# Kernel optimization log

Hardware: AMD Instinct MI355X
Metric: run time of the kernel (lower is better)

Reference implementation:

```python
import jax, jax.numpy as jnp
import numpy as np

D_MODEL = 2048
H_TOTAL = 32
D_HEAD = D_MODEL // H_TOTAL  # 64
H_ACTIVE = 4
ROPE_BASE = 10000.0


def _apply_rope(t, cos, sin):
    # t: [B, H, T, DH]; cos/sin: [T, DH//2]; interleaved pair rotation
    t1 = t[..., 0::2]
    t2 = t[..., 1::2]
    r1 = t1 * cos - t2 * sin
    r2 = t1 * sin + t2 * cos
    return jnp.stack([r1, r2], axis=-1).reshape(t.shape)


def setup_inputs() -> dict:
    key = jax.random.key(0)
    ks = jax.random.split(key, 4)
    x = jax.random.normal(ks[0], (4, 1024, D_MODEL), dtype=jnp.float32)
    w_router = jax.random.normal(ks[1], (D_MODEL, H_TOTAL), dtype=jnp.float32) * 0.02
    w_qkv = jax.random.normal(ks[2], (D_MODEL, 3 * D_MODEL), dtype=jnp.float32) * 0.02
    w_out = jax.random.normal(ks[3], (D_MODEL, D_MODEL), dtype=jnp.float32) * 0.02
    return {"x": x, "w_router": w_router, "w_qkv": w_qkv, "w_out": w_out}


def reference(x, w_router, w_qkv, w_out):
    B, T, _ = x.shape
    # --- SwitchRouter: per-token probabilities over heads ---
    probs = jax.nn.softmax(x @ w_router, axis=-1)            # [B, T, H]
    # top-h_active heads per token (dense-math equivalent of sparse dispatch)
    _, top_idx = jax.lax.top_k(probs, H_ACTIVE)              # [B, T, HA]
    mask = jnp.sum(jax.nn.one_hot(top_idx, H_TOTAL, dtype=x.dtype), axis=-2)  # [B, T, H]
    gate = probs * mask                                      # router-scored gate

    # --- QKV projection ---
    qkv = x @ w_qkv                                          # [B, T, 3D]
    q, k, v = jnp.split(qkv, 3, axis=-1)
    def to_heads(t):
        return t.reshape(B, T, H_TOTAL, D_HEAD).transpose(0, 2, 1, 3)  # [B, H, T, DH]
    q, k, v = to_heads(q), to_heads(k), to_heads(v)

    # --- RoPE ---
    inv_freq = 1.0 / (ROPE_BASE ** (jnp.arange(0, D_HEAD, 2, dtype=jnp.float32) / D_HEAD))
    ang = jnp.arange(T, dtype=jnp.float32)[:, None] * inv_freq[None, :]  # [T, DH/2]
    cos, sin = jnp.cos(ang), jnp.sin(ang)
    q = _apply_rope(q, cos, sin)
    k = _apply_rope(k, cos, sin)

    # --- causal SDPA ---
    scores = jnp.einsum('bhqd,bhkd->bhqk', q, k) / np.float32(np.sqrt(D_HEAD))
    causal = jnp.tril(jnp.ones((T, T), dtype=bool))
    scores = jnp.where(causal, scores, jnp.finfo(scores.dtype).min)
    attn = jax.nn.softmax(scores, axis=-1)
    out = jnp.einsum('bhqk,bhkd->bhqd', attn, v)             # [B, H, T, DH]

    # --- gate: only active heads contribute (scatter-back equivalent) ---
    out = out * gate.transpose(0, 2, 1)[..., None]           # [B, H, T, DH]
    out = out.transpose(0, 2, 1, 3).reshape(B, T, D_MODEL)
    return out @ w_out
```

## Files before the change

kernel.cpp:

```cpp
#include <hip/hip_runtime.h>
#include <hip/hip_bf16.h>
#include <stdint.h>
#include <stddef.h>

typedef __attribute__((ext_vector_type(8))) short bf16x8;
typedef __attribute__((ext_vector_type(8))) unsigned short u16x8;
typedef __attribute__((ext_vector_type(4))) float f32x4;
typedef __attribute__((ext_vector_type(16))) float f32x16;

#define TT 1024

__device__ __forceinline__ unsigned short f2bf(float f){
  unsigned u = __builtin_bit_cast(unsigned, f);
  unsigned r = 0x7fffu + ((u >> 16) & 1u);
  return (unsigned short)((u + r) >> 16);
}
__device__ __forceinline__ float bf2f(unsigned short s){
  unsigned u = ((unsigned)s) << 16;
  return __builtin_bit_cast(float, u);
}
__device__ __forceinline__ void gload16(const unsigned short* g, unsigned short* l){
  __builtin_amdgcn_global_load_lds(
      (const __attribute__((address_space(1))) void*)g,
      (__attribute__((address_space(3))) void*)l, 16, 0, 0);
}

#define MFMA32(a, b, c) __builtin_amdgcn_mfma_f32_32x32x16_bf16((a), (b), (c), 0, 0, 0)
#define MFMA_B16(a, b, c) __builtin_amdgcn_mfma_f32_16x16x32_bf16((a), (b), (c), 0, 0, 0)

__global__ void transpose_w_kernel(const float* __restrict__ wqkv, const float* __restrict__ wout,
                                   unsigned short* __restrict__ wqkvT, unsigned short* __restrict__ woutT){
  __shared__ float tile[32][33];
  const float* in; unsigned short* out; int C;
  int bx = blockIdx.x;
  if (bx < 192){ in = wqkv; out = wqkvT; C = 6144; }
  else         { in = wout; out = woutT; C = 2048; bx -= 192; }
  const int R = 2048;
  int c0 = bx * 32, r0 = blockIdx.y * 32;
  for (int i = threadIdx.y; i < 32; i += 8)
    tile[i][threadIdx.x] = in[(size_t)(r0 + i) * C + c0 + threadIdx.x];
  __syncthreads();
  for (int i = threadIdx.y; i < 32; i += 8)
    out[(size_t)(c0 + i) * R + r0 + threadIdx.x] = f2bf(tile[threadIdx.x][i]);
}

__global__ __launch_bounds__(256) void prep_kernel(const float* __restrict__ x,
                                                   const float* __restrict__ wr,
                                                   unsigned short* __restrict__ x_bf,
                                                   float* __restrict__ gate,
                                                   unsigned char* __restrict__ heads4,
                                                   float* __restrict__ tab){
  __shared__ float xc[8 * 256];
  __shared__ float red[8 * 8 * 32];
  const int tid = threadIdx.x;
  const int tok0 = blockIdx.x * 8;
  const int p = tid >> 5, h = tid & 31;

  if (blockIdx.x < 128){
    int i2 = blockIdx.x * 256 + tid;
    int pos = i2 >> 5, ii = i2 & 31;
    float freq = powf(10000.0f, -(float)ii / 32.0f);
    float ang = (float)pos * freq;
    tab[i2 * 2]     = cosf(ang);
    tab[i2 * 2 + 1] = sinf(ang);
  }

  float acc[8] = {0.f,0.f,0.f,0.f,0.f,0.f,0.f,0.f};
  for (int kb = 0; kb < 8; kb++){
    __syncthreads();
    {
      int tok = tid >> 5, e = (tid & 31) * 8;
      const float* xp = x + (size_t)(tok0 + tok) * 2048 + kb * 256 + e;
      float4 v0 = *(const float4*)xp, v1 = *(const float4*)(xp + 4);
      float vals[8] = {v0.x, v0.y, v0.z, v0.w, v1.x, v1.y, v1.z, v1.w};
      u16x8 ob;
      #pragma unroll
      for (int jj = 0; jj < 8; jj++) ob[jj] = f2bf(vals[jj]);
      *(u16x8*)(x_bf + (size_t)(tok0 + tok) * 2048 + kb * 256 + e) = ob;
      #pragma unroll
      for (int jj = 0; jj < 8; jj++) xc[tok * 256 + e + jj] = vals[jj];
    }
    __syncthreads();
    const float* wp = wr + (size_t)(kb * 256 + p * 32) * 32 + h;
    #pragma unroll 4
    for (int j = 0; j < 32; j++){
      float wv = wp[j * 32];
      #pragma unroll
      for (int tok = 0; tok < 8; tok++)
        acc[tok] += xc[tok * 256 + p * 32 + j] * wv;
    }
  }
  #pragma unroll
  for (int tok = 0; tok < 8; tok++) red[(p * 8 + tok) * 32 + h] = acc[tok];
  __syncthreads();
  {
    int lane = tid & 63;
    int tok = (tid >> 6) * 2 + (lane >> 5);
    int hh = lane & 31;
    float logit = 0.f;
    #pragma unroll
    for (int pp = 0; pp < 8; pp++) logit += red[(pp * 8 + tok) * 32 + hh];
    float m = logit;
    #pragma unroll
    for (int s = 16; s >= 1; s >>= 1) m = fmaxf(m, __shfl_xor(m, s));
    float e = __expf(logit - m);
    float sum = e;
    #pragma unroll
    for (int s = 16; s >= 1; s >>= 1) sum += __shfl_xor(sum, s);
    float prob = e / sum;
    float v = logit; int sel = 0;
    #pragma unroll
    for (int rr2 = 0; rr2 < 4; rr2++){
      float bv = v; int bi = hh;
      #pragma unroll
      for (int s = 16; s >= 1; s >>= 1){
        float ov = __shfl_xor(bv, s); int oi = __shfl_xor(bi, s);
        if (ov > bv || (ov == bv && oi < bi)) { bv = ov; bi = oi; }
      }
      if (hh == bi) { sel = 1; v = -3.4e38f; }
    }
    gate[(size_t)(tok0 + tok) * 32 + hh] = sel ? prob : 0.f;
    unsigned long long bal = __ballot(sel != 0);
    unsigned selmask = (unsigned)(bal >> ((lane >> 5) * 32));
    if (sel){
      int r = __popc(selmask & ((1u << hh) - 1u));
      heads4[(size_t)(tok0 + tok) * 4 + r] = (unsigned char)hh;
    }
  }
}

__global__ void compact_kernel(const unsigned char* __restrict__ heads4,
                               unsigned short* __restrict__ idx, int* __restrict__ counts){
  int bh = blockIdx.x;
  int b = bh >> 5, h = bh & 31;
  int lane = threadIdx.x;
  int base = 0;
  for (int c = 0; c < 16; c++){
    int t = c * 64 + lane;
    unsigned u = ((const unsigned*)heads4)[b * 1024 + t];
    int r = -1;
    if (((u      ) & 255) == (unsigned)h) r = 0;
    else if (((u >>  8) & 255) == (unsigned)h) r = 1;
    else if (((u >> 16) & 255) == (unsigned)h) r = 2;
    else if (((u >> 24) & 255) == (unsigned)h) r = 3;
    bool act = (r >= 0);
    unsigned long long mask = __ballot(act);
    int pos = base + __popcll(mask & ((1ull << lane) - 1ull));
    if (act) idx[bh * 1024 + pos] = (unsigned short)(t | (r << 10));
    base += __popcll(mask);
  }
  if (lane == 0) counts[bh] = base;
}

__global__ __launch_bounds__(256) void qgemm_kernel(const unsigned short* __restrict__ x_bf,
                                                    const unsigned short* __restrict__ wqkvT,
                                                    const unsigned short* __restrict__ idx,
                                                    const int* __restrict__ counts,
                                                    const float* __restrict__ tab,
                                                    unsigned short* __restrict__ qact){
  __shared__ float red[4][64][64];
  const int bh = blockIdx.x, qt = blockIdx.y;
  const int count = counts[bh];
  if (qt * 64 >= count) return;
  const int b = bh >> 5, h = bh & 31;
  const int tid = threadIdx.x, lane = tid & 63, w = tid >> 6;
  const int li = lane & 15, lg = lane >> 4;
  const int nvalid = min(64, count - qt * 64);
  const unsigned short* myidx = idx + bh * 1024 + qt * 64;

  int atok[4];
  #pragma unroll
  for (int ai = 0; ai < 4; ai++){
    int s = ai * 16 + li;
    atok[ai] = (s < nvalid) ? (myidx[s] & 1023) : 0;
  }
  const unsigned short* Bbase = wqkvT + (size_t)(h * 64) * 2048;

  f32x4 acc[4][4];
  #pragma unroll
  for (int i = 0; i < 4; i++)
    #pragma unroll
    for (int j = 0; j < 4; j++) acc[i][j] = f32x4{0.f, 0.f, 0.f, 0.f};

  const int k0w = w * 512;
  #pragma unroll 2
  for (int ks = 0; ks < 16; ks++){
    int k0 = k0w + ks * 32 + lg * 8;
    bf16x8 af[4], bw[4];
    #pragma unroll
    for (int ai = 0; ai < 4; ai++)
      af[ai] = *(const bf16x8*)(x_bf + (size_t)(b * 1024 + atok[ai]) * 2048 + k0);
    #pragma unroll
    for (int ni = 0; ni < 4; ni++)
      bw[ni] = *(const bf16x8*)(Bbase + (size_t)(ni * 16 + li) * 2048 + k0);
    #pragma unroll
    for (int ai = 0; ai < 4; ai++)
      #pragma unroll
      for (int ni = 0; ni < 4; ni++)
        acc[ai][ni] = MFMA_B16(af[ai], bw[ni], acc[ai][ni]);
  }
  #pragma unroll
  for (int ai = 0; ai < 4; ai++)
    #pragma unroll
    for (int ni = 0; ni < 4; ni++)
      #pragma unroll
      for (int rr = 0; rr < 4; rr++)
        red[w][ai * 16 + lg * 4 + rr][ni * 16 + li] = acc[ai][ni][rr];
  __syncthreads();

  int q = tid >> 2, dbase = (tid & 3) * 16;
  if (q < nvalid){
    int e = myidx[q];
    int tok = e & 1023, r = e >> 10;
    unsigned short* op = qact + ((size_t)((b << 10) + tok) * 4 + r) * 64;
    const float* tp = tab + ((size_t)tok * 32 + (dbase >> 1)) * 2;
    #pragma unroll
    for (int p = 0; p < 8; p++){
      int d0 = dbase + 2 * p;
      float v0 = red[0][q][d0] + red[1][q][d0] + red[2][q][d0] + red[3][q][d0];
      float v1 = red[0][q][d0 + 1] + red[1][q][d0 + 1] + red[2][q][d0 + 1] + red[3][q][d0 + 1];
      float c = tp[2 * p], s = tp[2 * p + 1];
      op[d0]     = f2bf(v0 * c - v1 * s);
      op[d0 + 1] = f2bf(v0 * s + v1 * c);
    }
  }
}

template<int MREP, int EPI>
__global__ __launch_bounds__(256, 2) void gemmk(const unsigned short* __restrict__ A,
                                                const unsigned short* __restrict__ Bt,
                                                float* __restrict__ Cf,
                                                unsigned short* __restrict__ kbuf,
                                                unsigned short* __restrict__ vt,
                                                const float* __restrict__ tab,
                                                int N, int K, int nbm){
  extern __shared__ unsigned short smem[];
  constexpr int BM = MREP * 64;
  constexpr int AU = MREP * 2048;
  constexpr int SLOT = AU + 4096;
  const int nblk = gridDim.x;
  const int raw = blockIdx.x;
  const int tile = (raw & 7) * (nblk >> 3) + (raw >> 3);
  const int bn = tile / nbm, bm = tile % nbm;

  const int tid = threadIdx.x, lane = tid & 63, wid = tid >> 6;
  const int wrow = wid >> 1, wcol = wid & 1;
  const int l31 = lane & 31, hi = lane >> 5;
  const int X = ((l31 >> 1) & 7) << 4;

  const unsigned short* gA[MREP];
  const unsigned short* gB[2];
  #pragma unroll
  for (int p = 0; p < MREP; p++){
    int L = tid * 16 + p * 4096;
    int line = L >> 7;
    int cs = (L & 127) ^ ((line & 7) << 4);
    gA[p] = A + (size_t)(bm * BM + line * 2 + (cs >> 6)) * K + ((cs & 63) >> 1);
  }
  #pragma unroll
  for (int p = 0; p < 2; p++){
    int L = tid * 16 + p * 4096;
    int line = L >> 7;
    int cs = (L & 127) ^ ((line & 7) << 4);
    gB[p] = Bt + (size_t)(bn * 128 + line * 2 + (cs >> 6)) * K + ((cs & 63) >> 1);
  }

  f32x16 acc[MREP][2];
  #pragma unroll
  for (int i = 0; i < MREP; i++)
    #pragma unroll
    for (int j = 0; j < 2; j++) acc[i][j] = f32x16{0,0,0,0,0,0,0,0,0,0,0,0,0,0,0,0};

  const int NT = K >> 5;
  #pragma unroll
  for (int tt = 0; tt < 2; tt++){
    unsigned short* sb = smem + tt * SLOT;
    #pragma unroll
    for (int p = 0; p < MREP; p++) gload16(gA[p] + (size_t)tt * 32, sb + tid * 8 + p * 2048);
    #pragma unroll
    for (int p = 0; p < 2; p++)    gload16(gB[p] + (size_t)tt * 32, sb + AU + tid * 8 + p * 2048);
  }

  for (int t = 0; t < NT; ++t){
    if (t < NT - 1){
      if constexpr (MREP == 4) asm volatile("s_waitcnt vmcnt(6)" ::: "memory");
      else                     asm volatile("s_waitcnt vmcnt(4)" ::: "memory");
    } else                     asm volatile("s_waitcnt vmcnt(0)" ::: "memory");
    __builtin_amdgcn_s_barrier();
    __builtin_amdgcn_sched_barrier(0);
    const unsigned short* bs = smem + (t % 3) * SLOT;
    unsigned short* ns = smem + ((t + 2) % 3) * SLOT;
    const bool st = (t + 2 < NT);
    #pragma unroll
    for (int ks = 0; ks < 2; ks++){
      const int bo = (((l31 & 1) * 64 + ks * 32 + hi * 16) ^ X) >> 1;
      bf16x8 av[MREP], bv[2];
      #pragma unroll
      for (int i = 0; i < MREP; i++)
        av[i] = *(const bf16x8*)(bs + (wrow * (MREP * 16) + i * 16 + (l31 >> 1)) * 64 + bo);
      #pragma unroll
      for (int j = 0; j < 2; j++)
        bv[j] = *(const bf16x8*)(bs + AU + (wcol * 32 + j * 16 + (l31 >> 1)) * 64 + bo);
      if (st){
        if (ks == 0){
          #pragma unroll
          for (int p = 0; p < MREP / 2 + 1; p++)
            gload16(gA[p] + (size_t)(t + 2) * 32, ns + tid * 8 + p * 2048);
        } else {
          #pragma unroll
          for (int p = MREP / 2 + 1; p < MREP; p++)
            gload16(gA[p] + (size_t)(t + 2) * 32, ns + tid * 8 + p * 2048);
          #pragma unroll
          for (int p = 0; p < 2; p++)
            gload16(gB[p] + (size_t)(t + 2) * 32, ns + AU + tid * 8 + p * 2048);
        }
      }
      #pragma unroll
      for (int i = 0; i < MREP; i++){
        acc[i][0] = MFMA32(av[i], bv[0], acc[i][0]);
        acc[i][1] = MFMA32(av[i], bv[1], acc[i][1]);
      }
    }
  }

  if constexpr (EPI == 1){
    if (bn < 16){
      #pragma unroll
      for (int i = 0; i < MREP; i++){
        #pragma unroll
        for (int j = 0; j < 2; j++){
          int col = bn * 128 + wcol * 64 + j * 32 + l31;
          int ii = (col & 63) >> 1;
          #pragma unroll
          for (int g = 0; g < 4; g++){
            #pragma unroll
            for (int rr = 0; rr < 4; rr++){
              int row = bm * BM + wrow * (BM / 2) + i * 32 + g * 8 + hi * 4 + rr;
              int pos = row & (TT - 1);
              const float* tp = tab + ((size_t)pos * 32 + ii) * 2;
              float c = tp[0], s = tp[1];
              float val = acc[i][j][g * 4 + rr];
              float pv = __shfl_xor(val, 1);
              float res = (lane & 1) ? (pv * s + val * c) : (val * c - pv * s);
              kbuf[(size_t)row * 2048 + col] = f2bf(res);
            }
          }
        }
      }
    } else {
      #pragma unroll
      for (int i = 0; i < MREP; i++){
        #pragma unroll
        for (int j = 0; j < 2; j++){
          int vcol = bn * 128 + wcol * 64 + j * 32 + l31 - 2048;
          int hh = vcol >> 6, d = vcol & 63;
          int row0 = bm * BM + wrow * (BM / 2) + i * 32 + hi * 4;
          int b = row0 >> 10, t0 = row0 & (TT - 1);
          #pragma unroll
          for (int g = 0; g < 4; g++){
            ushort4 pk;
            pk.x = f2bf(acc[i][j][g * 4 + 0]); pk.y = f2bf(acc[i][j][g * 4 + 1]);
            pk.z = f2bf(acc[i][j][g * 4 + 2]); pk.w = f2bf(acc[i][j][g * 4 + 3]);
            *(ushort4*)(vt + ((size_t)((b * 32 + hh) * 64 + d)) * TT + t0 + g * 8) = pk;
          }
        }
      }
    }
  } else {
    #pragma unroll
    for (int i = 0; i < MREP; i++){
      #pragma unroll
      for (int j = 0; j < 2; j++){
        int col = bn * 128 + wcol * 64 + j * 32 + l31;
        #pragma unroll
        for (int g = 0; g < 4; g++){
          #pragma unroll
          for (int rr = 0; rr < 4; rr++){
            size_t row = (size_t)(bm * BM + wrow * (BM / 2) + i * 32 + g * 8 + hi * 4 + rr);
            Cf[row * N + col] = acc[i][j][g * 4 + rr];
          }
        }
      }
    }
  }
}

__global__ __launch_bounds__(256) void attn_sparse_kernel(const unsigned short* __restrict__ qact,
                                                          const unsigned short* __restrict__ kbuf,
                                                          const unsigned short* __restrict__ vt,
                                                          const float* __restrict__ gate,
                                                          const unsigned short* __restrict__ idx,
                                                          const int* __restrict__ counts,
                                                          unsigned short* __restrict__ attn_out){
  __shared__ unsigned short Ks[64 * 64];
  __shared__ unsigned short Vs[64 * 64];
  __shared__ unsigned short Ps[4][16 * 64];
  const int bh = blockIdx.x, qt = blockIdx.y;
  const int count = counts[bh];
  if (qt * 64 >= count) return;
  const int b = bh >> 5, h = bh & 31;
  const int tid = threadIdx.x, lane = tid & 63, w = tid >> 6;
  const int li = lane & 15, lg = lane >> 4;
  const unsigned short* myidx = idx + bh * 1024 + qt * 64;
  const int nvalid = min(64, count - qt * 64);
  const int qmax = myidx[nvalid - 1] & 1023;

  int qi[4];
  #pragma unroll
  for (int r = 0; r < 4; r++){
    int s = w * 16 + lg * 4 + r;
    qi[r] = (s < nvalid) ? (myidx[s] & 1023) : -1;
  }
  bf16x8 qf0, qf1;
  {
    int s = w * 16 + li;
    int e2 = (s < nvalid) ? myidx[s] : 0;
    const unsigned short* qp = qact + ((size_t)((b << 10) + (e2 & 1023)) * 4 + (e2 >> 10)) * 64;
    qf0 = *(const bf16x8*)(qp + lg * 8);
    qf1 = *(const bf16x8*)(qp + 32 + lg * 8);
  }
  f32x4 o[4];
  #pragma unroll
  for (int i = 0; i < 4; i++) o[i] = f32x4{0.f, 0.f, 0.f, 0.f};
  float m_run[4], l_run[4];
  #pragma unroll
  for (int r = 0; r < 4; r++){ m_run[r] = -1e30f; l_run[r] = 0.f; }

  const int nkt = (qmax >> 6) + 1;
  for (int kt = 0; kt < nkt; kt++){
    const int kb = kt * 64;
    #pragma unroll
    for (int s2 = 0; s2 < 2; s2++){
      int s = s2 * 256 + tid;
      int r = s >> 3, c = (s & 7) * 8;
      gload16(kbuf + (size_t)(b * TT + kb + r) * 2048 + h * 64 + c, &Ks[s * 8]);
      gload16(vt + (size_t)(bh * 64 + r) * TT + kb + c, &Vs[s * 8]);
    }
    __syncthreads();

    f32x4 s4[4];
    #pragma unroll
    for (int ni = 0; ni < 4; ni++){
      bf16x8 k0 = *(const bf16x8*)(&Ks[(ni * 16 + li) * 64 + lg * 8]);
      bf16x8 k1 = *(const bf16x8*)(&Ks[(ni * 16 + li) * 64 + 32 + lg * 8]);
      f32x4 t = f32x4{0.f, 0.f, 0.f, 0.f};
      t = MFMA_B16(qf0, k0, t);
      t = MFMA_B16(qf1, k1, t);
      s4[ni] = t;
    }
    float mt[4];
    #pragma unroll
    for (int r = 0; r < 4; r++) mt[r] = -1e30f;
    #pragma unroll
    for (int ni = 0; ni < 4; ni++){
      int kidx = kb + ni * 16 + li;
      #pragma unroll
      for (int r = 0; r < 4; r++){
        float val = s4[ni][r] * 0.125f;
        val = (kidx <= qi[r]) ? val : -1e30f;
        s4[ni][r] = val;
        mt[r] = fmaxf(mt[r], val);
      }
    }
    #pragma unroll
    for (int r = 0; r < 4; r++){
      #pragma unroll
      for (int sh = 8; sh >= 1; sh >>= 1) mt[r] = fmaxf(mt[r], __shfl_xor(mt[r], sh));
      float mnew = fmaxf(m_run[r], mt[r]);
      float corr = __expf(m_run[r] - mnew);
      m_run[r] = mnew;
      l_run[r] *= corr;
      #pragma unroll
      for (int j = 0; j < 4; j++) o[j][r] *= corr;
    }
    float rs[4] = {0.f, 0.f, 0.f, 0.f};
    #pragma unroll
    for (int ni = 0; ni < 4; ni++)
      #pragma unroll
      for (int r = 0; r < 4; r++){
        float p = __expf(s4[ni][r] - m_run[r]);
        s4[ni][r] = p;
        rs[r] += p;
      }
    #pragma unroll
    for (int r = 0; r < 4; r++){
      #pragma unroll
      for (int sh = 8; sh >= 1; sh >>= 1) rs[r] += __shfl_xor(rs[r], sh);
      l_run[r] += rs[r];
    }
    #pragma unroll
    for (int ni = 0; ni < 4; ni++)
      #pragma unroll
      for (int r = 0; r < 4; r++)
        Ps[w][(lg * 4 + r) * 64 + ni * 16 + li] = f2bf(s4[ni][r]);
    #pragma unroll
    for (int ks = 0; ks < 2; ks++){
      bf16x8 pa = *(const bf16x8*)(&Ps[w][li * 64 + ks * 32 + lg * 8]);
      #pragma unroll
      for (int ni = 0; ni < 4; ni++){
        bf16x8 vb = *(const bf16x8*)(&Vs[(ni * 16 + li) * 64 + ks * 32 + lg * 8]);
        o[ni] = MFMA_B16(pa, vb, o[ni]);
      }
    }
    __syncthreads();
  }
  #pragma unroll
  for (int r = 0; r < 4; r++){
    if (qi[r] < 0) continue;
    float g = gate[(size_t)(b * TT + qi[r]) * 32 + h];
    float inv = g / l_run[r];
    #pragma unroll
    for (int ni = 0; ni < 4; ni++)
      attn_out[(size_t)(b * TT + qi[r]) * 2048 + h * 64 + ni * 16 + li] = f2bf(o[ni][r] * inv);
  }
}

extern "C" void kernel_launch(void* const* d_in, const int* in_sizes, int n_in,
                              void* d_out, int out_size, void* d_ws, size_t ws_size,
                              hipStream_t stream){
  const float* x        = (const float*)d_in[0];
  const float* w_router = (const float*)d_in[1];
  const float* w_qkv    = (const float*)d_in[2];
  const float* w_out    = (const float*)d_in[3];
  float* out = (float*)d_out;
  char* ws = (char*)d_ws;

  unsigned short* kbuf   = (unsigned short*)(ws);
  unsigned short* vt     = (unsigned short*)(ws + 16777216);
  unsigned short* qact   = (unsigned short*)(ws + 33554432);
  unsigned short* idx    = (unsigned short*)(ws + 37748736);
  int* counts            = (int*)(ws + 38010880);
  unsigned char* heads4  = (unsigned char*)(ws + 38011392);
  unsigned short* x_bf   = (unsigned short*)(ws + 50331648);
  unsigned short* wqkvT  = (unsigned short*)(ws + 67108864);
  unsigned short* woutT  = (unsigned short*)(ws + 92274688);
  float* gate            = (float*)(ws + 100663296);
  float* tab             = (float*)(ws + 101187584);
  unsigned short* attn   = x_bf;

  constexpr int KV_LDS  = 3 * (4 * 4096 + 8192) * 2 / 2;
  (void)hipFuncSetAttribute(reinterpret_cast<const void*>(&gemmk<4, 1>),
                            hipFuncAttributeMaxDynamicSharedMemorySize, KV_LDS);
  (void)hipFuncSetAttribute(reinterpret_cast<const void*>(&gemmk<4, 0>),
                            hipFuncAttributeMaxDynamicSharedMemorySize, KV_LDS);

  hipLaunchKernelGGL(transpose_w_kernel, dim3(256, 64), dim3(32, 8), 0, stream, w_qkv, w_out, wqkvT, woutT);
  hipLaunchKernelGGL(prep_kernel, dim3(512), dim3(256), 0, stream, x, w_router, x_bf, gate, heads4, tab);
  hipLaunchKernelGGL(compact_kernel, dim3(128), dim3(64), 0, stream, heads4, idx, counts);
  hipLaunchKernelGGL((gemmk<4, 1>), dim3(512), dim3(256), KV_LDS, stream,
                     x_bf, wqkvT + (size_t)2048 * 2048, (float*)nullptr, kbuf, vt, tab, 4096, 2048, 16);
  hipLaunchKernelGGL(qgemm_kernel, dim3(128, 16), dim3(256), 0, stream,
                     x_bf, wqkvT, idx, counts, tab, qact);
  (void)hipMemsetAsync(attn, 0, (size_t)4096 * 2048 * 2, stream);
  hipLaunchKernelGGL(attn_sparse_kernel, dim3(128, 16), dim3(256), 0, stream,
                     qact, kbuf, vt, gate, idx, counts, attn);
  hipLaunchKernelGGL((gemmk<4, 0>), dim3(256), dim3(256), KV_LDS, stream,
                     attn, woutT, out, (unsigned short*)nullptr, (unsigned short*)nullptr,
                     (const float*)nullptr, 2048, 2048, 16);
}
```

Measured before the change: 260.6 us.

## Replace dense output projection with sparse per-head GEMM and rank-partial reduce

The dense output projection over the full zero-padded attention buffer, together with its memset, is replaced. Attention results are now written in place into the compact qact buffer. A new kernel multiplies each active head's 64-wide slice by the matching W_out columns and writes bf16 partials into four rank-indexed buffers. A reduce kernel then sums those into the fp32 output. This skips the work for inactive heads (4 of 32) but adds the traffic of writing four bf16 partial tensors and reading them back, plus an extra rounding to bf16 before the sum.

Result: no change. 259.7 us (-0.3%).

```diff
diff --git a/kernel.cpp b/kernel.cpp
--- a/kernel.cpp
+++ b/kernel.cpp
@@ -226,15 +226,14 @@
   }
 }
 
-template<int MREP, int EPI>
 __global__ __launch_bounds__(256, 2) void gemmk(const unsigned short* __restrict__ A,
                                                 const unsigned short* __restrict__ Bt,
-                                                float* __restrict__ Cf,
                                                 unsigned short* __restrict__ kbuf,
                                                 unsigned short* __restrict__ vt,
                                                 const float* __restrict__ tab,
-                                                int N, int K, int nbm){
+                                                int K, int nbm){
   extern __shared__ unsigned short smem[];
+  constexpr int MREP = 4;
   constexpr int BM = MREP * 64;
   constexpr int AU = MREP * 2048;
   constexpr int SLOT = AU + 4096;
@@ -282,10 +281,8 @@
   }
 
   for (int t = 0; t < NT; ++t){
-    if (t < NT - 1){
-      if constexpr (MREP == 4) asm volatile("s_waitcnt vmcnt(6)" ::: "memory");
-      else                     asm volatile("s_waitcnt vmcnt(4)" ::: "memory");
-    } else                     asm volatile("s_waitcnt vmcnt(0)" ::: "memory");
+    if (t < NT - 1) asm volatile("s_waitcnt vmcnt(6)" ::: "memory");
+    else            asm volatile("s_waitcnt vmcnt(0)" ::: "memory");
     __builtin_amdgcn_s_barrier();
     __builtin_amdgcn_sched_barrier(0);
     const unsigned short* bs = smem + (t % 3) * SLOT;
@@ -304,12 +301,10 @@
       if (st){
         if (ks == 0){
           #pragma unroll
-          for (int p = 0; p < MREP / 2 + 1; p++)
+          for (int p = 0; p < 3; p++)
             gload16(gA[p] + (size_t)(t + 2) * 32, ns + tid * 8 + p * 2048);
         } else {
-          #pragma unroll
-          for (int p = MREP / 2 + 1; p < MREP; p++)
-            gload16(gA[p] + (size_t)(t + 2) * 32, ns + tid * 8 + p * 2048);
+          gload16(gA[3] + (size_t)(t + 2) * 32, ns + tid * 8 + 3 * 2048);
           #pragma unroll
           for (int p = 0; p < 2; p++)
             gload16(gB[p] + (size_t)(t + 2) * 32, ns + AU + tid * 8 + p * 2048);
@@ -323,75 +318,56 @@
     }
   }
 
-  if constexpr (EPI == 1){
-    if (bn < 16){
-      #pragma unroll
-      for (int i = 0; i < MREP; i++){
-        #pragma unroll
-        for (int j = 0; j < 2; j++){
-          int col = bn * 128 + wcol * 64 + j * 32 + l31;
-          int ii = (col & 63) >> 1;
-          #pragma unroll
-          for (int g = 0; g < 4; g++){
-            #pragma unroll
-            for (int rr = 0; rr < 4; rr++){
-              int row = bm * BM + wrow * (BM / 2) + i * 32 + g * 8 + hi * 4 + rr;
-              int pos = row & (TT - 1);
-              const float* tp = tab + ((size_t)pos * 32 + ii) * 2;
-              float c = tp[0], s = tp[1];
-              float val = acc[i][j][g * 4 + rr];
-              float pv = __shfl_xor(val, 1);
-              float res = (lane & 1) ? (pv * s + val * c) : (val * c - pv * s);
-              kbuf[(size_t)row * 2048 + col] = f2bf(res);
-            }
-          }
-        }
-      }
-    } else {
-      #pragma unroll
-      for (int i = 0; i < MREP; i++){
-        #pragma unroll
-        for (int j = 0; j < 2; j++){
-          int vcol = bn * 128 + wcol * 64 + j * 32 + l31 - 2048;
-          int hh = vcol >> 6, d = vcol & 63;
-          int row0 = bm * BM + wrow * (BM / 2) + i * 32 + hi * 4;
-          int b = row0 >> 10, t0 = row0 & (TT - 1);
-          #pragma unroll
-          for (int g = 0; g < 4; g++){
-            ushort4 pk;
-            pk.x = f2bf(acc[i][j][g * 4 + 0]); pk.y = f2bf(acc[i][j][g * 4 + 1]);
-            pk.z = f2bf(acc[i][j][g * 4 + 2]); pk.w = f2bf(acc[i][j][g * 4 + 3]);
-            *(ushort4*)(vt + ((size_t)((b * 32 + hh) * 64 + d)) * TT + t0 + g * 8) = pk;
-          }
-        }
-      }
-    }
-  } else {
+  if (bn < 16){
     #pragma unroll
     for (int i = 0; i < MREP; i++){
       #pragma unroll
       for (int j = 0; j < 2; j++){
         int col = bn * 128 + wcol * 64 + j * 32 + l31;
+        int ii = (col & 63) >> 1;
         #pragma unroll
         for (int g = 0; g < 4; g++){
           #pragma unroll
           for (int rr = 0; rr < 4; rr++){
-            size_t row = (size_t)(bm * BM + wrow * (BM / 2) + i * 32 + g * 8 + hi * 4 + rr);
-            Cf[row * N + col] = acc[i][j][g * 4 + rr];
+            int row = bm * BM + wrow * (BM / 2) + i * 32 + g * 8 + hi * 4 + rr;
+            int pos = row & (TT - 1);
+            const float* tp = tab + ((size_t)pos * 32 + ii) * 2;
+            float c = tp[0], s = tp[1];
+            float val = acc[i][j][g * 4 + rr];
+            float pv = __shfl_xor(val, 1);
+            float res = (lane & 1) ? (pv * s + val * c) : (val * c - pv * s);
+            kbuf[(size_t)row * 2048 + col] = f2bf(res);
           }
         }
       }
     }
-  }
-}
-
-__global__ __launch_bounds__(256) void attn_sparse_kernel(const unsigned short* __restrict__ qact,
+  } else {
+    #pragma unroll
+    for (int i = 0; i < MREP; i++){
+      #pragma unroll
+      for (int j = 0; j < 2; j++){
+        int vcol = bn * 128 + wcol * 64 + j * 32 + l31 - 2048;
+        int hh = vcol >> 6, d = vcol & 63;
+        int row0 = bm * BM + wrow * (BM / 2) + i * 32 + hi * 4;
+        int b = row0 >> 10, t0 = row0 & (TT - 1);
+        #pragma unroll
+        for (int g = 0; g < 4; g++){
+          ushort4 pk;
+          pk.x = f2bf(acc[i][j][g * 4 + 0]); pk.y = f2bf(acc[i][j][g * 4 + 1]);
+          pk.z = f2bf(acc[i][j][g * 4 + 2]); pk.w = f2bf(acc[i][j][g * 4 + 3]);
+          *(ushort4*)(vt + ((size_t)((b * 32 + hh) * 64 + d)) * TT + t0 + g * 8) = pk;
+        }
+      }
+    }
+  }
+}
+
+__global__ __launch_bounds__(256) void attn_sparse_kernel(unsigned short* __restrict__ qact,
                                                           const unsigned short* __restrict__ kbuf,
                                                           const unsigned short* __restrict__ vt,
                                                           const float* __restrict__ gate,
                                                           const unsigned short* __restrict__ idx,
-                                                          const int* __restrict__ counts,
-                                                          unsigned short* __restrict__ attn_out){
+                                                          const int* __restrict__ counts){
   __shared__ unsigned short Ks[64 * 64];
   __shared__ unsigned short Vs[64 * 64];
   __shared__ unsigned short Ps[4][16 * 64];
@@ -509,10 +485,102 @@
     if (qi[r] < 0) continue;
     float g = gate[(size_t)(b * TT + qi[r]) * 32 + h];
     float inv = g / l_run[r];
+    int e = myidx[w * 16 + lg * 4 + r];
+    unsigned short* op = qact + ((size_t)((b << 10) + (e & 1023)) * 4 + (e >> 10)) * 64;
     #pragma unroll
     for (int ni = 0; ni < 4; ni++)
-      attn_out[(size_t)(b * TT + qi[r]) * 2048 + h * 64 + ni * 16 + li] = f2bf(o[ni][r] * inv);
-  }
+      op[ni * 16 + li] = f2bf(o[ni][r] * inv);
+  }
+}
+
+__global__ __launch_bounds__(256) void outsp_kernel(const unsigned short* __restrict__ qact,
+                                                    const unsigned short* __restrict__ woutT,
+                                                    const unsigned short* __restrict__ idx,
+                                                    const int* __restrict__ counts,
+                                                    unsigned short* __restrict__ p0,
+                                                    unsigned short* __restrict__ p1,
+                                                    unsigned short* __restrict__ p2,
+                                                    unsigned short* __restrict__ p3){
+  __shared__ unsigned short As[64 * 64];
+  __shared__ unsigned short sidx[64];
+  const int bh = blockIdx.x, qt = blockIdx.y;
+  const int count = counts[bh];
+  if (qt * 64 >= count) return;
+  const int b = bh >> 5, h = bh & 31;
+  const int tid = threadIdx.x, lane = tid & 63, w = tid >> 6;
+  const int li = lane & 15, lg = lane >> 4;
+  const int nvalid = min(64, count - qt * 64);
+  const unsigned short* myidx = idx + bh * 1024 + qt * 64;
+
+  if (tid < 64) sidx[tid] = myidx[(tid < nvalid) ? tid : 0];
+  #pragma unroll
+  for (int s2 = 0; s2 < 2; s2++){
+    int s = s2 * 256 + tid;
+    int row = s >> 3, bc = (s & 7) * 16;
+    int e = myidx[(row < nvalid) ? row : 0];
+    const unsigned short* src = qact + ((size_t)((b << 10) + (e & 1023)) * 4 + (e >> 10)) * 64;
+    gload16(src + ((bc ^ ((row & 7) << 4)) >> 1), &As[s * 8]);
+  }
+  __syncthreads();
+
+  const int kX = (li & 7) << 4;
+  const int n0w = w * 512;
+  #pragma unroll 2
+  for (int nc = 0; nc < 8; nc++){
+    const int n0 = n0w + nc * 64;
+    f32x4 acc[4][4];
+    #pragma unroll
+    for (int i = 0; i < 4; i++)
+      #pragma unroll
+      for (int j = 0; j < 4; j++) acc[i][j] = f32x4{0.f, 0.f, 0.f, 0.f};
+    bf16x8 bfr[4][2];
+    #pragma unroll
+    for (int ni = 0; ni < 4; ni++)
+      #pragma unroll
+      for (int kh = 0; kh < 2; kh++)
+        bfr[ni][kh] = *(const bf16x8*)(woutT + (size_t)(n0 + ni * 16 + li) * 2048 + h * 64 + kh * 32 + lg * 8);
+    #pragma unroll
+    for (int ti = 0; ti < 4; ti++){
+      bf16x8 a0 = *(const bf16x8*)(&As[((ti * 16 + li) * 128 + ((lg * 16) ^ kX)) >> 1]);
+      bf16x8 a1 = *(const bf16x8*)(&As[((ti * 16 + li) * 128 + ((64 + lg * 16) ^ kX)) >> 1]);
+      #pragma unroll
+      for (int ni = 0; ni < 4; ni++){
+        acc[ti][ni] = MFMA_B16(a0, bfr[ni][0], acc[ti][ni]);
+        acc[ti][ni] = MFMA_B16(a1, bfr[ni][1], acc[ti][ni]);
+      }
+    }
+    #pragma unroll
+    for (int ti = 0; ti < 4; ti++){
+      #pragma unroll
+      for (int rr = 0; rr < 4; rr++){
+        int slot = ti * 16 + lg * 4 + rr;
+        if (slot < nvalid){
+          int e = sidx[slot];
+          int tok = e & 1023, rk = e >> 10;
+          unsigned short* pp = (rk == 0) ? p0 : (rk == 1) ? p1 : (rk == 2) ? p2 : p3;
+          size_t base = (size_t)(b * 1024 + tok) * 2048 + n0;
+          #pragma unroll
+          for (int ni = 0; ni < 4; ni++)
+            pp[base + ni * 16 + li] = f2bf(acc[ti][ni][rr]);
+        }
+      }
+    }
+  }
+}
+
+__global__ void reduce_kernel(const unsigned short* __restrict__ p0,
+                              const unsigned short* __restrict__ p1,
+                              const unsigned short* __restrict__ p2,
+                              const unsigned short* __restrict__ p3,
+                              float* __restrict__ out){
+  size_t i = ((size_t)blockIdx.x * 256 + threadIdx.x) * 8;
+  u16x8 a = *(const u16x8*)(p0 + i);
+  u16x8 b = *(const u16x8*)(p1 + i);
+  u16x8 c = *(const u16x8*)(p2 + i);
+  u16x8 d = *(const u16x8*)(p3 + i);
+  #pragma unroll
+  for (int j = 0; j < 8; j++)
+    out[i + j] = bf2f(a[j]) + bf2f(b[j]) + bf2f(c[j]) + bf2f(d[j]);
 }
 
 extern "C" void kernel_launch(void* const* d_in, const int* in_sizes, int n_in,
@@ -536,25 +604,26 @@
   unsigned short* woutT  = (unsigned short*)(ws + 92274688);
   float* gate            = (float*)(ws + 100663296);
   float* tab             = (float*)(ws + 101187584);
-  unsigned short* attn   = x_bf;
-
-  constexpr int KV_LDS  = 3 * (4 * 4096 + 8192) * 2 / 2;
-  (void)hipFuncSetAttribute(reinterpret_cast<const void*>(&gemmk<4, 1>),
-                            hipFuncAttributeMaxDynamicSharedMemorySize, KV_LDS);
-  (void)hipFuncSetAttribute(reinterpret_cast<const void*>(&gemmk<4, 0>),
+  unsigned short* part0  = kbuf;
+  unsigned short* part1  = vt;
+  unsigned short* part2  = x_bf;
+  unsigned short* part3  = wqkvT;
+
+  constexpr int KV_LDS = 3 * (4 * 4096 + 8192) * 2 / 2;
+  (void)hipFuncSetAttribute(reinterpret_cast<const void*>(&gemmk),
                             hipFuncAttributeMaxDynamicSharedMemorySize, KV_LDS);
 
   hipLaunchKernelGGL(transpose_w_kernel, dim3(256, 64), dim3(32, 8), 0, stream, w_qkv, w_out, wqkvT, woutT);
   hipLaunchKernelGGL(prep_kernel, dim3(512), dim3(256), 0, stream, x, w_router, x_bf, gate, heads4, tab);
   hipLaunchKernelGGL(compact_kernel, dim3(128), dim3(64), 0, stream, heads4, idx, counts);
-  hipLaunchKernelGGL((gemmk<4, 1>), dim3(512), dim3(256), KV_LDS, stream,
-                     x_bf, wqkvT + (size_t)2048 * 2048, (float*)nullptr, kbuf, vt, tab, 4096, 2048, 16);
+  hipLaunchKernelGGL(gemmk, dim3(512), dim3(256), KV_LDS, stream,
+                     x_bf, wqkvT + (size_t)2048 * 2048, kbuf, vt, tab, 2048, 16);
   hipLaunchKernelGGL(qgemm_kernel, dim3(128, 16), dim3(256), 0, stream,
                      x_bf, wqkvT, idx, counts, tab, qact);
-  (void)hipMemsetAsync(attn, 0, (size_t)4096 * 2048 * 2, stream);
   hipLaunchKernelGGL(attn_sparse_kernel, dim3(128, 16), dim3(256), 0, stream,
-                     qact, kbuf, vt, gate, idx, counts, attn);
-  hipLaunchKernelGGL((gemmk<4, 0>), dim3(256), dim3(256), KV_LDS, stream,
-                     attn, woutT, out, (unsigned short*)nullptr, (unsigned short*)nullptr,
-                     (const float*)nullptr, 2048, 2048, 16);
-}
+                     qact, kbuf, vt, gate, idx, counts);
+  hipLaunchKernelGGL(outsp_kernel, dim3(128, 16), dim3(256), 0, stream,
+                     qact, woutT, idx, counts, part0, part1, part2, part3);
+  hipLaunchKernelGGL(reduce_kernel, dim3(4096), dim3(256), 0, stream,
+                     part0, part1, part2, part3, out);
+}
```
